# Performance work log

Measured on AMD Instinct MI355X. Metric: run time of the kernel, lower is better.

## Reference

```python
import jax, jax.numpy as jnp
import numpy as np

B, N, QD, ED, H, DH = 2, 512, 512, 11, 4, 64
INNER = H * DH
SCALE = DH ** -0.5


def setup_inputs() -> dict:
    key = jax.random.key(0)
    ks = jax.random.split(key, 16)
    s = 0.02
    x = jax.random.normal(ks[0], (B, N, QD), jnp.float32)
    mask = jax.random.randint(ks[1], (B, N, N), 0, 2).astype(bool)
    mask = mask | jnp.eye(N, dtype=bool)[None]  # ensure each row attends somewhere
    edge_attr = jax.random.normal(ks[2], (B, N, N, ED), jnp.float32)
    return {
        "x": x,
        "adjacency_mask": mask,
        "edge_attr": edge_attr,
        "Wq": jax.random.normal(ks[3], (QD, INNER), jnp.float32) * s,
        "Wk": jax.random.normal(ks[4], (QD, INNER), jnp.float32) * s,
        "Wv": jax.random.normal(ks[5], (QD, INNER), jnp.float32) * s,
        "Web1": jax.random.normal(ks[6], (ED, INNER), jnp.float32) * s,
        "beb1": jnp.zeros((INNER,), jnp.float32),
        "Web2": jax.random.normal(ks[7], (INNER, H), jnp.float32) * s,
        "beb2": jnp.zeros((H,), jnp.float32),
        "Wev1": jax.random.normal(ks[8], (ED, INNER), jnp.float32) * s,
        "bev1": jnp.zeros((INNER,), jnp.float32),
        "Wev2": jax.random.normal(ks[9], (INNER, INNER), jnp.float32) * s,
        "bev2": jnp.zeros((INNER,), jnp.float32),
        "Wo": jax.random.normal(ks[10], (INNER, QD), jnp.float32) * s,
        "bo": jnp.zeros((QD,), jnp.float32),
    }


def reference(x, adjacency_mask, edge_attr, Wq, Wk, Wv, Web1, beb1, Web2, beb2,
              Wev1, bev1, Wev2, bev2, Wo, bo):
    b, n, _ = x.shape
    # project and split heads: b n (h d) -> b h n d
    def heads(t):
        return t.reshape(b, n, H, DH).transpose(0, 2, 1, 3)
    q = heads(x @ Wq)
    k = heads(x @ Wk)
    v = heads(x @ Wv)

    # edge bias MLP: [b,i,j,ed] -> [b,i,j,h] -> [b,h,i,j]  (exact GELU, matching torch default)
    eb_h = jax.nn.gelu(edge_attr @ Web1 + beb1, approximate=False)
    edge_bias = (eb_h @ Web2 + beb2).transpose(0, 3, 1, 2)
    # edge value MLP: [b,i,j,ed] -> [b,i,j,inner] -> [b,h,i,j,d]
    ev_h = jax.nn.gelu(edge_attr @ Wev1 + bev1, approximate=False)
    edge_value = (ev_h @ Wev2 + bev2).reshape(b, n, n, H, DH).transpose(0, 3, 1, 2, 4)

    sim = jnp.einsum('bhid,bhjd->bhij', q, k) * SCALE + edge_bias
    neg = -jnp.finfo(sim.dtype).max
    sim = jnp.where(adjacency_mask[:, None, :, :], sim, neg)
    attn = jax.nn.softmax(sim, axis=-1)

    # out = sum_j attn * (v_j + edge_value_ij) = attn@v + einsum over edge_value
    out = jnp.einsum('bhij,bhjd->bhid', attn, v) \
        + jnp.einsum('bhij,bhijd->bhid', attn, edge_value)
    out = out.transpose(0, 2, 1, 3).reshape(b, n, INNER)
    return out @ Wo + bo, attn
```

## Files before the change

kernel.cpp:

```cpp
#include <hip/hip_runtime.h>
#include <hip/hip_bf16.h>
#include <math.h>

#define NB 2
#define NN 512
#define QD 512
#define ED 11
#define NH 4
#define DH 64
#define INNER 256
#define SCALE 0.125f
#define NEGMAX -3.402823466e38f

typedef const __hip_bfloat16* bfp;
typedef float f32x2 __attribute__((ext_vector_type(2)));
typedef __attribute__((ext_vector_type(4))) float f32x4;
typedef __attribute__((ext_vector_type(4))) short s16x4;

template<int FM>
__device__ __forceinline__ float ldf(const void* p, size_t i) {
    if (FM) return ((const float*)p)[i];
    return __bfloat162float(((bfp)p)[i]);
}

__device__ __forceinline__ unsigned short f2bf(float x) {
    __hip_bfloat16 h = __float2bfloat16(x);
    return __builtin_bit_cast(unsigned short, h);
}

template<int FM>
__device__ __forceinline__ unsigned short ldb(const void* p, size_t i) {
    if (FM) return f2bf(((const float*)p)[i]);
    return ((const unsigned short*)p)[i];
}

__device__ __forceinline__ f32x4 mfma16(s16x4 a, s16x4 b, f32x4 c) {
    return __builtin_amdgcn_mfma_f32_16x16x16bf16_1k(a, b, c, 0, 0, 0);
}

#define QKV_F   (NB*NN*768)
#define OIN_F   (NB*NN*INNER)
#define OFF_QKV   0
#define OFF_OIN   (OFF_QKV + QKV_F)
#define OFF_FLAGS (OFF_OIN + OIN_F)
#define OFF_KBF   (OFF_FLAGS + 4)
#define OFF_WPK   (OFF_KBF + 131072)
#define OFF_WOPK  (OFF_WPK + 196608)

__device__ __forceinline__ f32x2 pkfma(f32x2 a, f32x2 b, f32x2 c) {
    return __builtin_elementwise_fma(a, b, c);
}
__device__ __forceinline__ f32x2 mk2(float x, float y) { f32x2 r; r.x = x; r.y = y; return r; }
__device__ __forceinline__ f32x2 bc2(float x) { f32x2 r; r.x = x; r.y = x; return r; }
__device__ __forceinline__ f32x4 bc4(float x) { f32x4 r; r.x = x; r.y = x; r.z = x; r.w = x; return r; }

__device__ __forceinline__ f32x2 gelu2(f32x2 x) {
    f32x2 t = x * x;
    f32x2 p = pkfma(t, bc2(-0.0023746715f), bc2(0.019947114f));
    p = pkfma(t, p, bc2(-0.13298076f));
    p = pkfma(t, p, bc2(0.7978845608f));
    return x * pkfma(bc2(0.5f) * x, p, bc2(0.5f));
}

__device__ __forceinline__ s16x4 gelu_pack(f32x4 d) {
    f32x2 glo = gelu2(mk2(d.x, d.y));
    f32x2 ghi = gelu2(mk2(d.z, d.w));
    s16x4 b;
    b.x = (short)f2bf(glo.x); b.y = (short)f2bf(glo.y);
    b.z = (short)f2bf(ghi.x); b.w = (short)f2bf(ghi.y);
    return b;
}

__device__ __forceinline__ bool maskAt(int mode, const void* p, size_t idx) {
    switch (mode) {
        case 0:  return ((const int*)p)[idx] != 0;
        case 1:  return ((const unsigned char*)p)[idx] != 0;
        case 2:  return ((const unsigned short*)p)[idx] != 0;
        default: return ((const float*)p)[idx] != 0.0f;
    }
}

__global__ void detect_modes(const void* x, const void* mask, int* flags) {
    __shared__ int sh_f32, sh_i32ok, sh_u8ok;
    if (threadIdx.x == 0) { sh_f32 = 0; sh_i32ok = 1; sh_u8ok = 1; }
    __syncthreads();
    const unsigned short* hx = (const unsigned short*)x;
    int f32hit = 0;
    for (int i = threadIdx.x; i < 4096; i += 256) {
        unsigned e = (hx[i] >> 7) & 0xFFu;
        if (e >= 0xC0u) f32hit = 1;
    }
    if (f32hit) atomicOr(&sh_f32, 1);
    const unsigned int* pm = (const unsigned int*)mask;
    int bad_i = 0, bad_b = 0;
    for (int i = threadIdx.x; i < 1024; i += 256) {
        unsigned v = pm[i];
        if (v > 1u) bad_i = 1;
        if ((v & 255u) > 1u || ((v >> 8) & 255u) > 1u ||
            ((v >> 16) & 255u) > 1u || ((v >> 24) & 255u) > 1u) bad_b = 1;
    }
    if (bad_i) atomicAnd(&sh_i32ok, 0);
    if (bad_b) atomicAnd(&sh_u8ok, 0);
    __syncthreads();
    if (threadIdx.x == 0) {
        flags[0] = sh_f32;
        int mm;
        if (sh_i32ok) mm = 0;
        else if (sh_u8ok) mm = 1;
        else mm = (((const unsigned short*)mask)[0] != 0) ? 2 : 3;
        flags[1] = mm;
    }
}

template<int FM>
__global__ __launch_bounds__(256) void pack_w_kernel(
        const void* Wq, const void* Wk, const void* Wv, const void* Wo,
        const int* flags, unsigned short* wpk, unsigned short* wopk) {
    if (flags[0] != FM) return;
    const int id = blockIdx.x * 256 + threadIdx.x;
    if (id < 98304) {
        const int c = id % 768, a = id / 768;
        const void* W = (c < 256) ? Wq : ((c < 512) ? Wk : Wv);
        const int cc = c & 255;
        unsigned short* dst = wpk + ((size_t)a * 768 + c) * 4;
#pragma unroll
        for (int e = 0; e < 4; e++)
            dst[e] = ldb<FM>(W, (size_t)(4 * a + e) * INNER + cc);
    } else {
        const int id2 = id - 98304;
        const int c = id2 % 512, a = id2 / 512;
        unsigned short* dst = wopk + ((size_t)a * 512 + c) * 4;
#pragma unroll
        for (int e = 0; e < 4; e++)
            dst[e] = ldb<FM>(Wo, (size_t)(4 * a + e) * QD + c);
    }
}

template<int FM>
__global__ __launch_bounds__(256) void qkv_mfma_kernel(
        const void* x, const int* flags, const unsigned short* wpk,
        float* qkv, unsigned short* kbf) {
    if (flags[0] != FM) return;
    __shared__ unsigned short xs[16 * 520];
    const int rb  = blockIdx.x / 12;
    const int cgq = blockIdx.x % 12;
    const int r0 = rb * 16;
    const int t = threadIdx.x;
    const int lane = t & 63, wave = t >> 6;
    const int lj = lane & 15, g = lane >> 4;
    for (int idx = t; idx < 16 * 512; idx += 256) {
        int r = idx >> 9, c = idx & 511;
        xs[r * 520 + c] = ldb<FM>(x, (size_t)(r0 + r) * QD + c);
    }
    __syncthreads();
    const int cb = cgq * 64 + wave * 16;
    f32x4 acc = {0.f, 0.f, 0.f, 0.f};
#pragma unroll 8
    for (int ks = 0; ks < 32; ks++) {
        s16x4 a = *(const s16x4*)&xs[lj * 520 + ks * 16 + 4 * g];
        s16x4 b = *(const s16x4*)&wpk[((size_t)(ks * 4 + g) * 768 + cb + lj) * 4];
        acc = mfma16(a, b, acc);
    }
    const int col = cb + lj;
#pragma unroll
    for (int e = 0; e < 4; e++) {
        const int row = r0 + 4 * g + e;
        float v = acc[e];
        qkv[(size_t)row * 768 + col] = v;
        if (col >= 256 && col < 512) kbf[(size_t)row * 256 + (col - 256)] = f2bf(v);
    }
}

template<int FM>
__global__ __launch_bounds__(256) void outproj_mfma_kernel(
        const float* oin, const unsigned short* wopk, const void* bo,
        const int* flags, void* d_out) {
    if (flags[0] != FM) return;
    __shared__ unsigned short os[16 * 264];
    const int rb  = blockIdx.x >> 3;
    const int cgq = blockIdx.x & 7;
    const int r0 = rb * 16;
    const int t = threadIdx.x;
    const int lane = t & 63, wave = t >> 6;
    const int lj = lane & 15, g = lane >> 4;
    for (int idx = t; idx < 16 * 256; idx += 256) {
        int r = idx >> 8, c = idx & 255;
        os[r * 264 + c] = f2bf(oin[(size_t)(r0 + r) * INNER + c]);
    }
    __syncthreads();
    const int cb = cgq * 64 + wave * 16;
    f32x4 acc = {0.f, 0.f, 0.f, 0.f};
#pragma unroll
    for (int ks = 0; ks < 16; ks++) {
        s16x4 a = *(const s16x4*)&os[lj * 264 + ks * 16 + 4 * g];
        s16x4 b = *(const s16x4*)&wopk[((size_t)(ks * 4 + g) * 512 + cb + lj) * 4];
        acc = mfma16(a, b, acc);
    }
    const int col = cb + lj;
    const float bv = ldf<FM>(bo, col);
#pragma unroll
    for (int e = 0; e < 4; e++) {
        const int row = r0 + 4 * g + e;
        float v = acc[e] + bv;
        if (FM) ((float*)d_out)[(size_t)row * QD + col] = v;
        else    ((__hip_bfloat16*)d_out)[(size_t)row * QD + col] = __float2bfloat16(v);
    }
}

#define SM_EA    0
#define SM_W1T   20480
#define SM_WV1T  30720
#define SM_W2T   40960
#define SM_QST   43072
#define SM_JLIST 45184
#define SM_CTL   46208
#define SM_SIMT  46272
#define SM_TOTAL 54464

template<int FM>
__global__ __launch_bounds__(512, 4) void attn_ev_kernel(
        const void* ea, const void* mask,
        const void* Web1, const void* beb1, const void* Web2, const void* beb2,
        const void* Wev1, const void* bev1, const void* Wev2, const void* bev2,
        const int* flags, const float* qkv, const unsigned short* kbf,
        float* oin, void* d_out) {
    if (flags[0] != FM) return;
    const int mmode = flags[1];
    __shared__ __align__(16) char smem_raw[SM_TOTAL];
    unsigned short* ea_s  = (unsigned short*)(smem_raw + SM_EA);
    unsigned short* w1t   = (unsigned short*)(smem_raw + SM_W1T);
    unsigned short* wv1t  = (unsigned short*)(smem_raw + SM_WV1T);
    unsigned short* w2t   = (unsigned short*)(smem_raw + SM_W2T);
    unsigned short* qst   = (unsigned short*)(smem_raw + SM_QST);
    unsigned short* jlist = (unsigned short*)(smem_raw + SM_JLIST);
    int* ctl              = (int*)(smem_raw + SM_CTL);
    float* simT           = (float*)(smem_raw + SM_SIMT);

    const int blk = blockIdx.x;
    const int b = blk >> 9, i = blk & (NN - 1);
    const int t = threadIdx.x;
    const int lane = t & 63, wave = t >> 6;
    const int lj = lane & 15;
    const int g  = lane >> 4;
    const f32x4 FZ = {0.f, 0.f, 0.f, 0.f};
    const size_t mrow = (size_t)(b * NN + i) * NN;

    {
        const size_t ea_row = (size_t)(b * NN + i) * (NN * ED);
        for (int idx = t; idx < NN * 16; idx += 512) {
            int j = idx >> 4, k = idx & 15;
            unsigned short v;
            if (k < ED)       v = ldb<FM>(ea, ea_row + j * ED + k);
            else if (k == ED) v = 0x3F80;
            else              v = 0;
            ea_s[j * 20 + k] = v;
        }
        for (int idx = t; idx < 256 * 16; idx += 512) {
            int c = idx >> 4, k = idx & 15;
            unsigned short v1 = 0, v2 = 0;
            if (k < ED) { v1 = ldb<FM>(Web1, (size_t)k * INNER + c);
                          v2 = ldb<FM>(Wev1, (size_t)k * INNER + c); }
            else if (k == ED) { v1 = ldb<FM>(beb1, c); v2 = ldb<FM>(bev1, c); }
            w1t[c * 20 + k]  = v1;
            wv1t[c * 20 + k] = v2;
        }
        const float* qrow = qkv + (size_t)(b * NN + i) * 768;
        for (int idx = t; idx < 4 * 256; idx += 512) {
            int h = idx >> 8, c = idx & 255;
            w2t[h * 264 + c] = ldb<FM>(Web2, (size_t)c * NH + h);
            qst[h * 264 + c] = ((c >> 6) == h) ? f2bf(qrow[c] * SCALE) : (unsigned short)0;
        }
        {
            float4 nf; nf.x = NEGMAX; nf.y = NEGMAX; nf.z = NEGMAX; nf.w = NEGMAX;
            *(float4*)&simT[t * 4] = nf;
        }
    }
    const bool um = maskAt(mmode, mask, mrow + t);
    const unsigned long long bal = __ballot(um);
    if (lane == 0) {
        ctl[wave] = __popcll(bal);
        unsigned long long nb = ~bal;
        ctl[8 + wave] = nb ? (wave * 64 + (int)__ffsll((long long)nb) - 1) : 0x7fffffff;
    }
    __syncthreads();

    int M, padJ;
    {
        int s = 0, mybase = 0, pj = 0x7fffffff;
#pragma unroll
        for (int w = 0; w < 8; w++) {
            if (w == wave) mybase = s;
            s += ctl[w];
            pj = min(pj, ctl[8 + w]);
        }
        M = s;
        padJ = (pj == 0x7fffffff) ? 0 : pj;
        if (um) jlist[mybase + __popcll(bal & ((1ull << lane) - 1ull))] = (unsigned short)t;
    }
    __syncthreads();
    const int T = (M + 15) >> 4;

    {
        float bb2v[4];
#pragma unroll
        for (int h = 0; h < 4; h++) bb2v[h] = ldf<FM>(beb2, h);
        const unsigned short* a2base = w2t + (lj & 3) * 264;
        const unsigned short* a3base = qst + (lj & 3) * 264;
        for (int tt = wave; tt < T; tt += 8) {
            const int sbase = tt * 16;
            const int slot = sbase + lj;
            const int jme = (slot < M) ? (int)jlist[slot] : padJ;
            const unsigned short* kbase = kbf + ((size_t)(b * NN) + jme) * 256;
            s16x4 kf0[8], kf1[8];
#pragma unroll
            for (int u = 0; u < 8; u++) kf0[u] = *(const s16x4*)&kbase[u * 16 + 4 * g];
            const s16x4 b1 = *(const s16x4*)&ea_s[jme * 20 + 4 * g];
            f32x4 accA = FZ;
#pragma unroll
            for (int hb = 0; hb < 2; hb++) {
                if (hb == 1) {
#pragma unroll
                    for (int u = 0; u < 8; u++)
                        kf1[u] = *(const s16x4*)&kbase[(8 + u) * 16 + 4 * g];
                }
                f32x4 d1s[8];
#pragma unroll
                for (int u = 0; u < 8; u++) {
                    s16x4 wa1 = *(const s16x4*)&w1t[((hb * 8 + u) * 16 + lj) * 20 + 4 * g];
                    d1s[u] = mfma16(wa1, b1, FZ);
                }
                __builtin_amdgcn_sched_barrier(0);
                s16x4 b2s[8];
#pragma unroll
                for (int u = 0; u < 8; u++) b2s[u] = gelu_pack(d1s[u]);
                __builtin_amdgcn_sched_barrier(0);
#pragma unroll
                for (int u = 0; u < 8; u++) {
                    s16x4 wa2 = *(const s16x4*)&a2base[(hb * 8 + u) * 16 + 4 * g];
                    accA = mfma16(wa2, b2s[u], accA);
                }
                __builtin_amdgcn_sched_barrier(0);
            }
            f32x4 accB0 = FZ, accB1 = FZ;
#pragma unroll
            for (int ct = 0; ct < 16; ct++) {
                s16x4 a3 = *(const s16x4*)&a3base[ct * 16 + 4 * g];
                s16x4 kv = (ct < 8) ? kf0[ct] : kf1[ct - 8];
                if (ct & 1) accB1 = mfma16(a3, kv, accB1);
                else        accB0 = mfma16(a3, kv, accB0);
            }
            if (lane < 16) {
                const int sl2 = sbase + lane;
                if (sl2 < M) {
                    const int j = (int)jlist[sl2];
                    float4 sv;
                    sv.x = accA.x + accB0.x + accB1.x + bb2v[0];
                    sv.y = accA.y + accB0.y + accB1.y + bb2v[1];
                    sv.z = accA.z + accB0.z + accB1.z + bb2v[2];
                    sv.w = accA.w + accB0.w + accB1.w + bb2v[3];
                    *(float4*)&simT[j * 4] = sv;
                }
            }
        }
    }
    __syncthreads();

    if (wave < NH) {
        const int h = wave;
        float sv[8], pv[8];
        float mx = NEGMAX;
#pragma unroll
        for (int it = 0; it < 8; it++) {
            sv[it] = simT[(lane + it * 64) * 4 + h];
            mx = fmaxf(mx, sv[it]);
        }
#pragma unroll
        for (int off = 1; off < 64; off <<= 1) mx = fmaxf(mx, __shfl_xor(mx, off, 64));
        float sum = 0.f;
#pragma unroll
        for (int it = 0; it < 8; it++) { pv[it] = __expf(sv[it] - mx); sum += pv[it]; }
#pragma unroll
        for (int off = 1; off < 64; off <<= 1) sum += __shfl_xor(sum, off, 64);
        float inv = 1.0f / sum;
        size_t base = (size_t)NB * NN * QD + ((size_t)(b * NH + h) * NN + i) * NN;
#pragma unroll
        for (int it = 0; it < 8; it++) {
            float a = pv[it] * inv;
            simT[(lane + it * 64) * 4 + h] = a;
            if (FM) ((float*)d_out)[base + lane + it * 64] = a;
            else    ((__hip_bfloat16*)d_out)[base + lane + it * 64] = __float2bfloat16(a);
        }
    }
    __syncthreads();

    f32x4 awacc[4];
#pragma unroll
    for (int cc = 0; cc < 4; cc++) awacc[cc] = FZ;
    f32x4 avp4 = FZ;
    const int jhalf = wave >> 2, cq = wave & 3;
    {
        s16x4 b1r[4];
#pragma unroll
        for (int cc = 0; cc < 4; cc++)
            b1r[cc] = *(const s16x4*)&wv1t[((cq * 4 + cc) * 16 + lj) * 20 + 4 * g];
        const int h4 = lj & 3;
        for (int tt = jhalf; tt < T; tt += 2) {
            const int sbase = tt * 16;
            const int slotm = sbase + lj;
            const int jm = (slotm < M) ? (int)jlist[slotm] : padJ;
            const s16x4 a1 = *(const s16x4*)&ea_s[jm * 20 + 4 * g];
            s16x4 a2;
            {
                const int s0 = sbase + 4 * g;
                const int ja = (s0 + 0 < M) ? (int)jlist[s0 + 0] : padJ;
                const int jb = (s0 + 1 < M) ? (int)jlist[s0 + 1] : padJ;
                const int jc = (s0 + 2 < M) ? (int)jlist[s0 + 2] : padJ;
                const int jd = (s0 + 3 < M) ? (int)jlist[s0 + 3] : padJ;
                a2.x = (short)f2bf(simT[ja * 4 + h4]);
                a2.y = (short)f2bf(simT[jb * 4 + h4]);
                a2.z = (short)f2bf(simT[jc * 4 + h4]);
                a2.w = (short)f2bf(simT[jd * 4 + h4]);
            }
            f32x4 d1s[4];
#pragma unroll
            for (int cc = 0; cc < 4; cc++) d1s[cc] = mfma16(a1, b1r[cc], FZ);
            __builtin_amdgcn_sched_barrier(0);
            s16x4 b2s[4];
#pragma unroll
            for (int cc = 0; cc < 4; cc++) b2s[cc] = gelu_pack(d1s[cc]);
            __builtin_amdgcn_sched_barrier(0);
#pragma unroll
            for (int cc = 0; cc < 4; cc++)
                awacc[cc] = mfma16(a2, b2s[cc], awacc[cc]);
            __builtin_amdgcn_sched_barrier(0);
        }
        const float* vrow0 = qkv + (size_t)(b * NN) * 768 + 512;
        const int Mw = ((M + 63) & ~63) >> 3;
        const int s0w = wave * Mw;
        for (int sb = 0; sb < Mw; sb += 8) {
            float at8[8]; f32x4 vv[8];
#pragma unroll
            for (int u = 0; u < 8; u++) {
                const int slot = s0w + sb + u;
                const int j = (slot < M) ? (int)jlist[slot] : padJ;
                at8[u] = simT[j * 4 + g];
                vv[u] = *(const f32x4*)(vrow0 + (size_t)j * 768 + 4 * lane);
            }
#pragma unroll
            for (int u = 0; u < 8; u++)
                avp4 = __builtin_elementwise_fma(bc4(at8[u]), vv[u], avp4);
        }
    }
    __syncthreads();

    {
        float* pbufAW = (float*)smem_raw;
        float* pbufAV = (float*)smem_raw + 2048;
        if (lane < 16) {
#pragma unroll
            for (int cc = 0; cc < 4; cc++) {
                const int cbase = (cq * 4 + cc) * 16 + lane;
                pbufAW[jhalf * 1024 + 0 * 256 + cbase] = awacc[cc].x;
                pbufAW[jhalf * 1024 + 1 * 256 + cbase] = awacc[cc].y;
                pbufAW[jhalf * 1024 + 2 * 256 + cbase] = awacc[cc].z;
                pbufAW[jhalf * 1024 + 3 * 256 + cbase] = awacc[cc].w;
            }
        }
        *(float4*)&pbufAV[wave * 256 + 4 * lane] = *(float4*)&avp4;
        __syncthreads();
        float* accw = (float*)(smem_raw + SM_SIMT);
        for (int idx = t; idx < 1280; idx += 512) {
            if (idx < 1024) {
                accw[idx] = pbufAW[idx] + pbufAW[1024 + idx];
            } else {
                const int c = idx - 1024;
                float s = 0.f;
#pragma unroll
                for (int w = 0; w < 8; w++) s += pbufAV[w * 256 + c];
                accw[idx] = s;
            }
        }
    }
    __syncthreads();

    {
        const float* accw = (const float*)(smem_raw + SM_SIMT);
        float* pepi = (float*)(smem_raw + SM_SIMT) + 1280;
        const int c = t & 255;
        const int hh = c >> 6;
        const int half = t >> 8;
        float o = 0.f;
        const int cp0 = half * 128, cp1 = cp0 + 128;
        for (int cp = cp0; cp < cp1; cp += 4) {
            const float4 aw4 = *(const float4*)&accw[hh * 256 + cp];
            o = fmaf(aw4.x, ldf<FM>(Wev2, (size_t)(cp + 0) * INNER + c), o);
            o = fmaf(aw4.y, ldf<FM>(Wev2, (size_t)(cp + 1) * INNER + c), o);
            o = fmaf(aw4.z, ldf<FM>(Wev2, (size_t)(cp + 2) * INNER + c), o);
            o = fmaf(aw4.w, ldf<FM>(Wev2, (size_t)(cp + 3) * INNER + c), o);
        }
        pepi[t] = o;
        __syncthreads();
        if (t < 256) {
            float out_v = ldf<FM>(bev2, c) + accw[1024 + c] + pepi[c] + pepi[c + 256];
            oin[(size_t)(b * NN + i) * INNER + c] = out_v;
        }
    }
}

extern "C" void kernel_launch(void* const* d_in, const int* in_sizes, int n_in,
                              void* d_out, int out_size, void* d_ws, size_t ws_size,
                              hipStream_t stream) {
    (void)in_sizes; (void)n_in; (void)out_size; (void)ws_size;
    const void* x    = d_in[0];
    const void* mask = d_in[1];
    const void* ea   = d_in[2];
    const void* Wq   = d_in[3];
    const void* Wk   = d_in[4];
    const void* Wv   = d_in[5];
    const void* Web1 = d_in[6];
    const void* beb1 = d_in[7];
    const void* Web2 = d_in[8];
    const void* beb2 = d_in[9];
    const void* Wev1 = d_in[10];
    const void* bev1 = d_in[11];
    const void* Wev2 = d_in[12];
    const void* bev2 = d_in[13];
    const void* Wo   = d_in[14];
    const void* bo   = d_in[15];

    float* ws    = (float*)d_ws;
    float* qkv   = ws + OFF_QKV;
    float* oin   = ws + OFF_OIN;
    int*   flags = (int*)(ws + OFF_FLAGS);
    unsigned short* kbf  = (unsigned short*)(ws + OFF_KBF);
    unsigned short* wpk  = (unsigned short*)(ws + OFF_WPK);
    unsigned short* wopk = (unsigned short*)(ws + OFF_WOPK);

    detect_modes<<<1, 256, 0, stream>>>(x, mask, flags);

    pack_w_kernel<0><<<512, 256, 0, stream>>>(Wq, Wk, Wv, Wo, flags, wpk, wopk);
    pack_w_kernel<1><<<512, 256, 0, stream>>>(Wq, Wk, Wv, Wo, flags, wpk, wopk);

    qkv_mfma_kernel<0><<<768, 256, 0, stream>>>(x, flags, wpk, qkv, kbf);
    qkv_mfma_kernel<1><<<768, 256, 0, stream>>>(x, flags, wpk, qkv, kbf);

    attn_ev_kernel<0><<<NB * NN, 512, 0, stream>>>(ea, mask, Web1, beb1, Web2, beb2,
                                                   Wev1, bev1, Wev2, bev2,
                                                   flags, qkv, kbf, oin, d_out);
    attn_ev_kernel<1><<<NB * NN, 512, 0, stream>>>(ea, mask, Web1, beb1, Web2, beb2,
                                                   Wev1, bev1, Wev2, bev2,
                                                   flags, qkv, kbf, oin, d_out);

    outproj_mfma_kernel<0><<<512, 256, 0, stream>>>(oin, wopk, bo, flags, d_out);
    outproj_mfma_kernel<1><<<512, 256, 0, stream>>>(oin, wopk, bo, flags, d_out);
}
```

Measured before the change: 216.7 us.

## Fuse output projection into attention kernel and drop dual-dtype template launches

Each attention block now applies the Wo projection (plus bias) to its own output row in shared memory and writes the final output directly. This removes the separate outproj kernel and its intermediate global buffer. The compile-time FM template is replaced by a runtime flag read, which halves the number of kernel launches. The cost is that every block streams all of packed Wo and runs scalar FMAs instead of MFMA, and the runtime dtype branches may add a little overhead inside the kernels.

```diff
diff --git a/kernel.cpp b/kernel.cpp
--- a/kernel.cpp
+++ b/kernel.cpp
@@ -17,21 +17,19 @@
 typedef __attribute__((ext_vector_type(4))) float f32x4;
 typedef __attribute__((ext_vector_type(4))) short s16x4;
 
-template<int FM>
-__device__ __forceinline__ float ldf(const void* p, size_t i) {
-    if (FM) return ((const float*)p)[i];
-    return __bfloat162float(((bfp)p)[i]);
-}
-
 __device__ __forceinline__ unsigned short f2bf(float x) {
     __hip_bfloat16 h = __float2bfloat16(x);
     return __builtin_bit_cast(unsigned short, h);
 }
-
-template<int FM>
-__device__ __forceinline__ unsigned short ldb(const void* p, size_t i) {
-    if (FM) return f2bf(((const float*)p)[i]);
-    return ((const unsigned short*)p)[i];
+__device__ __forceinline__ float bfu2f(unsigned short u) {
+    return __builtin_bit_cast(float, (unsigned)u << 16);
+}
+
+__device__ __forceinline__ float ldf(int FM, const void* p, size_t i) {
+    return FM ? ((const float*)p)[i] : __bfloat162float(((bfp)p)[i]);
+}
+__device__ __forceinline__ unsigned short ldb(int FM, const void* p, size_t i) {
+    return FM ? f2bf(((const float*)p)[i]) : ((const unsigned short*)p)[i];
 }
 
 __device__ __forceinline__ f32x4 mfma16(s16x4 a, s16x4 b, f32x4 c) {
@@ -39,10 +37,8 @@
 }
 
 #define QKV_F   (NB*NN*768)
-#define OIN_F   (NB*NN*INNER)
 #define OFF_QKV   0
-#define OFF_OIN   (OFF_QKV + QKV_F)
-#define OFF_FLAGS (OFF_OIN + OIN_F)
+#define OFF_FLAGS (OFF_QKV + QKV_F)
 #define OFF_KBF   (OFF_FLAGS + 4)
 #define OFF_WPK   (OFF_KBF + 131072)
 #define OFF_WOPK  (OFF_WPK + 196608)
@@ -112,11 +108,10 @@
     }
 }
 
-template<int FM>
 __global__ __launch_bounds__(256) void pack_w_kernel(
         const void* Wq, const void* Wk, const void* Wv, const void* Wo,
         const int* flags, unsigned short* wpk, unsigned short* wopk) {
-    if (flags[0] != FM) return;
+    const int FM = flags[0];
     const int id = blockIdx.x * 256 + threadIdx.x;
     if (id < 98304) {
         const int c = id % 768, a = id / 768;
@@ -125,22 +120,21 @@
         unsigned short* dst = wpk + ((size_t)a * 768 + c) * 4;
 #pragma unroll
         for (int e = 0; e < 4; e++)
-            dst[e] = ldb<FM>(W, (size_t)(4 * a + e) * INNER + cc);
+            dst[e] = ldb(FM, W, (size_t)(4 * a + e) * INNER + cc);
     } else {
         const int id2 = id - 98304;
         const int c = id2 % 512, a = id2 / 512;
         unsigned short* dst = wopk + ((size_t)a * 512 + c) * 4;
 #pragma unroll
         for (int e = 0; e < 4; e++)
-            dst[e] = ldb<FM>(Wo, (size_t)(4 * a + e) * QD + c);
-    }
-}
-
-template<int FM>
+            dst[e] = ldb(FM, Wo, (size_t)(4 * a + e) * QD + c);
+    }
+}
+
 __global__ __launch_bounds__(256) void qkv_mfma_kernel(
         const void* x, const int* flags, const unsigned short* wpk,
         float* qkv, unsigned short* kbf) {
-    if (flags[0] != FM) return;
+    const int FM = flags[0];
     __shared__ unsigned short xs[16 * 520];
     const int rb  = blockIdx.x / 12;
     const int cgq = blockIdx.x % 12;
@@ -150,7 +144,7 @@
     const int lj = lane & 15, g = lane >> 4;
     for (int idx = t; idx < 16 * 512; idx += 256) {
         int r = idx >> 9, c = idx & 511;
-        xs[r * 520 + c] = ldb<FM>(x, (size_t)(r0 + r) * QD + c);
+        xs[r * 520 + c] = ldb(FM, x, (size_t)(r0 + r) * QD + c);
     }
     __syncthreads();
     const int cb = cgq * 64 + wave * 16;
@@ -168,42 +162,6 @@
         float v = acc[e];
         qkv[(size_t)row * 768 + col] = v;
         if (col >= 256 && col < 512) kbf[(size_t)row * 256 + (col - 256)] = f2bf(v);
-    }
-}
-
-template<int FM>
-__global__ __launch_bounds__(256) void outproj_mfma_kernel(
-        const float* oin, const unsigned short* wopk, const void* bo,
-        const int* flags, void* d_out) {
-    if (flags[0] != FM) return;
-    __shared__ unsigned short os[16 * 264];
-    const int rb  = blockIdx.x >> 3;
-    const int cgq = blockIdx.x & 7;
-    const int r0 = rb * 16;
-    const int t = threadIdx.x;
-    const int lane = t & 63, wave = t >> 6;
-    const int lj = lane & 15, g = lane >> 4;
-    for (int idx = t; idx < 16 * 256; idx += 256) {
-        int r = idx >> 8, c = idx & 255;
-        os[r * 264 + c] = f2bf(oin[(size_t)(r0 + r) * INNER + c]);
-    }
-    __syncthreads();
-    const int cb = cgq * 64 + wave * 16;
-    f32x4 acc = {0.f, 0.f, 0.f, 0.f};
-#pragma unroll
-    for (int ks = 0; ks < 16; ks++) {
-        s16x4 a = *(const s16x4*)&os[lj * 264 + ks * 16 + 4 * g];
-        s16x4 b = *(const s16x4*)&wopk[((size_t)(ks * 4 + g) * 512 + cb + lj) * 4];
-        acc = mfma16(a, b, acc);
-    }
-    const int col = cb + lj;
-    const float bv = ldf<FM>(bo, col);
-#pragma unroll
-    for (int e = 0; e < 4; e++) {
-        const int row = r0 + 4 * g + e;
-        float v = acc[e] + bv;
-        if (FM) ((float*)d_out)[(size_t)row * QD + col] = v;
-        else    ((__hip_bfloat16*)d_out)[(size_t)row * QD + col] = __float2bfloat16(v);
     }
 }
 
@@ -217,14 +175,13 @@
 #define SM_SIMT  46272
 #define SM_TOTAL 54464
 
-template<int FM>
 __global__ __launch_bounds__(512, 4) void attn_ev_kernel(
         const void* ea, const void* mask,
         const void* Web1, const void* beb1, const void* Web2, const void* beb2,
         const void* Wev1, const void* bev1, const void* Wev2, const void* bev2,
-        const int* flags, const float* qkv, const unsigned short* kbf,
-        float* oin, void* d_out) {
-    if (flags[0] != FM) return;
+        const void* bo, const int* flags, const float* qkv,
+        const unsigned short* kbf, const unsigned short* wopk, void* d_out) {
+    const int FM = flags[0];
     const int mmode = flags[1];
     __shared__ __align__(16) char smem_raw[SM_TOTAL];
     unsigned short* ea_s  = (unsigned short*)(smem_raw + SM_EA);
@@ -250,7 +207,7 @@
         for (int idx = t; idx < NN * 16; idx += 512) {
             int j = idx >> 4, k = idx & 15;
             unsigned short v;
-            if (k < ED)       v = ldb<FM>(ea, ea_row + j * ED + k);
+            if (k < ED)       v = ldb(FM, ea, ea_row + j * ED + k);
             else if (k == ED) v = 0x3F80;
             else              v = 0;
             ea_s[j * 20 + k] = v;
@@ -258,16 +215,16 @@
         for (int idx = t; idx < 256 * 16; idx += 512) {
             int c = idx >> 4, k = idx & 15;
             unsigned short v1 = 0, v2 = 0;
-            if (k < ED) { v1 = ldb<FM>(Web1, (size_t)k * INNER + c);
-                          v2 = ldb<FM>(Wev1, (size_t)k * INNER + c); }
-            else if (k == ED) { v1 = ldb<FM>(beb1, c); v2 = ldb<FM>(bev1, c); }
+            if (k < ED) { v1 = ldb(FM, Web1, (size_t)k * INNER + c);
+                          v2 = ldb(FM, Wev1, (size_t)k * INNER + c); }
+            else if (k == ED) { v1 = ldb(FM, beb1, c); v2 = ldb(FM, bev1, c); }
             w1t[c * 20 + k]  = v1;
             wv1t[c * 20 + k] = v2;
         }
         const float* qrow = qkv + (size_t)(b * NN + i) * 768;
         for (int idx = t; idx < 4 * 256; idx += 512) {
             int h = idx >> 8, c = idx & 255;
-            w2t[h * 264 + c] = ldb<FM>(Web2, (size_t)c * NH + h);
+            w2t[h * 264 + c] = ldb(FM, Web2, (size_t)c * NH + h);
             qst[h * 264 + c] = ((c >> 6) == h) ? f2bf(qrow[c] * SCALE) : (unsigned short)0;
         }
         {
@@ -303,7 +260,7 @@
     {
         float bb2v[4];
 #pragma unroll
-        for (int h = 0; h < 4; h++) bb2v[h] = ldf<FM>(beb2, h);
+        for (int h = 0; h < 4; h++) bb2v[h] = ldf(FM, beb2, h);
         const unsigned short* a2base = w2t + (lj & 3) * 264;
         const unsigned short* a3base = qst + (lj & 3) * 264;
         for (int tt = wave; tt < T; tt += 8) {
@@ -486,6 +443,7 @@
     {
         const float* accw = (const float*)(smem_raw + SM_SIMT);
         float* pepi = (float*)(smem_raw + SM_SIMT) + 1280;
+        float* orow = (float*)(smem_raw + SM_SIMT) + 1792;
         const int c = t & 255;
         const int hh = c >> 6;
         const int half = t >> 8;
@@ -493,17 +451,36 @@
         const int cp0 = half * 128, cp1 = cp0 + 128;
         for (int cp = cp0; cp < cp1; cp += 4) {
             const float4 aw4 = *(const float4*)&accw[hh * 256 + cp];
-            o = fmaf(aw4.x, ldf<FM>(Wev2, (size_t)(cp + 0) * INNER + c), o);
-            o = fmaf(aw4.y, ldf<FM>(Wev2, (size_t)(cp + 1) * INNER + c), o);
-            o = fmaf(aw4.z, ldf<FM>(Wev2, (size_t)(cp + 2) * INNER + c), o);
-            o = fmaf(aw4.w, ldf<FM>(Wev2, (size_t)(cp + 3) * INNER + c), o);
+            o = fmaf(aw4.x, ldf(FM, Wev2, (size_t)(cp + 0) * INNER + c), o);
+            o = fmaf(aw4.y, ldf(FM, Wev2, (size_t)(cp + 1) * INNER + c), o);
+            o = fmaf(aw4.z, ldf(FM, Wev2, (size_t)(cp + 2) * INNER + c), o);
+            o = fmaf(aw4.w, ldf(FM, Wev2, (size_t)(cp + 3) * INNER + c), o);
         }
         pepi[t] = o;
         __syncthreads();
         if (t < 256) {
-            float out_v = ldf<FM>(bev2, c) + accw[1024 + c] + pepi[c] + pepi[c + 256];
-            oin[(size_t)(b * NN + i) * INNER + c] = out_v;
-        }
+            orow[c] = ldf(FM, bev2, c) + accw[1024 + c] + pepi[c] + pepi[c + 256];
+        }
+    }
+    __syncthreads();
+
+    {
+        const float* orow = (const float*)(smem_raw + SM_SIMT) + 1792;
+        const int col = t;
+        float acc = ldf(FM, bo, col);
+        const unsigned short* wp = wopk + (size_t)col * 4;
+#pragma unroll 8
+        for (int a = 0; a < 64; a++) {
+            const s16x4 w4 = *(const s16x4*)(wp + (size_t)a * 512 * 4);
+            const float4 o4 = *(const float4*)&orow[a * 4];
+            acc = fmaf(o4.x, bfu2f((unsigned short)w4.x), acc);
+            acc = fmaf(o4.y, bfu2f((unsigned short)w4.y), acc);
+            acc = fmaf(o4.z, bfu2f((unsigned short)w4.z), acc);
+            acc = fmaf(o4.w, bfu2f((unsigned short)w4.w), acc);
+        }
+        const size_t row = (size_t)(b * NN + i);
+        if (FM) ((float*)d_out)[row * QD + col] = acc;
+        else    ((__hip_bfloat16*)d_out)[row * QD + col] = __float2bfloat16(acc);
     }
 }
 
@@ -530,7 +507,6 @@
 
     float* ws    = (float*)d_ws;
     float* qkv   = ws + OFF_QKV;
-    float* oin   = ws + OFF_OIN;
     int*   flags = (int*)(ws + OFF_FLAGS);
     unsigned short* kbf  = (unsigned short*)(ws + OFF_KBF);
     unsigned short* wpk  = (unsigned short*)(ws + OFF_WPK);
@@ -538,19 +514,11 @@
 
     detect_modes<<<1, 256, 0, stream>>>(x, mask, flags);
 
-    pack_w_kernel<0><<<512, 256, 0, stream>>>(Wq, Wk, Wv, Wo, flags, wpk, wopk);
-    pack_w_kernel<1><<<512, 256, 0, stream>>>(Wq, Wk, Wv, Wo, flags, wpk, wopk);
-
-    qkv_mfma_kernel<0><<<768, 256, 0, stream>>>(x, flags, wpk, qkv, kbf);
-    qkv_mfma_kernel<1><<<768, 256, 0, stream>>>(x, flags, wpk, qkv, kbf);
-
-    attn_ev_kernel<0><<<NB * NN, 512, 0, stream>>>(ea, mask, Web1, beb1, Web2, beb2,
-                                                   Wev1, bev1, Wev2, bev2,
-                                                   flags, qkv, kbf, oin, d_out);
-    attn_ev_kernel<1><<<NB * NN, 512, 0, stream>>>(ea, mask, Web1, beb1, Web2, beb2,
-                                                   Wev1, bev1, Wev2, bev2,
-                                                   flags, qkv, kbf, oin, d_out);
-
-    outproj_mfma_kernel<0><<<512, 256, 0, stream>>>(oin, wopk, bo, flags, d_out);
-    outproj_mfma_kernel<1><<<512, 256, 0, stream>>>(oin, wopk, bo, flags, d_out);
-}
+    pack_w_kernel<<<512, 256, 0, stream>>>(Wq, Wk, Wv, Wo, flags, wpk, wopk);
+
+    qkv_mfma_kernel<<<768, 256, 0, stream>>>(x, flags, wpk, qkv, kbf);
+
+    attn_ev_kernel<<<NB * NN, 512, 0, stream>>>(ea, mask, Web1, beb1, Web2, beb2,
+                                                Wev1, bev1, Wev2, bev2, bo,
+                                                flags, qkv, kbf, wopk, d_out);
+}
```

After: 236.4 us. 1.09x slower.
